# Performance work log

Measured on AMD Instinct MI355X. Metric: run time of the kernel, lower is better.

The kernel has to match this reference:

```python
import jax, jax.numpy as jnp
import numpy as np

B, T, D = 1, 2048, 2048
H, KVH, G, HD = 32, 8, 4, 64  # n_heads, n_kv_heads, n_groups, head_dim


def _rope_angles(t, hd):
    # standard RoPE angle table: [T, hd//2]
    inv_freq = 1.0 / (10000.0 ** (jnp.arange(0, hd, 2, dtype=jnp.float32) / hd))
    return jnp.arange(t, dtype=jnp.float32)[:, None] * inv_freq[None, :]


def setup_inputs() -> dict:
    key = jax.random.key(0)
    k1, k2, k3, k4, k5 = jax.random.split(key, 5)
    scale = 0.02
    return {
        "x": jax.random.normal(k1, (B, T, D), dtype=jnp.float32),
        "freqs": _rope_angles(T, HD),                                  # [T, HD//2]
        "wq": jax.random.normal(k2, (D, H * HD), dtype=jnp.float32) * scale,
        "wk": jax.random.normal(k3, (D, KVH * HD), dtype=jnp.float32) * scale,
        "wv": jax.random.normal(k4, (D, KVH * HD), dtype=jnp.float32) * scale,
        "wo": jax.random.normal(k5, (H * HD, D), dtype=jnp.float32) * scale,
    }


def _apply_rope(t, cos, sin):
    # t: [B, T, nh, HD]; cos/sin: [T, HD//2] -> broadcast [1, T, 1, HD//2]
    t1, t2 = t[..., ::2], t[..., 1::2]
    c = cos[None, :, None, :]
    s = sin[None, :, None, :]
    out_even = t1 * c - t2 * s
    out_odd = t1 * s + t2 * c
    return jnp.stack([out_even, out_odd], axis=-1).reshape(t.shape)


def reference(x, freqs, wq, wk, wv, wo):
    b, t, _ = x.shape
    q = (x @ wq).reshape(b, t, H, HD)
    k = (x @ wk).reshape(b, t, KVH, HD)
    v = (x @ wv).reshape(b, t, KVH, HD)

    cos, sin = jnp.cos(freqs), jnp.sin(freqs)
    q = _apply_rope(q, cos, sin)
    k = _apply_rope(k, cos, sin)

    # GQA: repeat_interleave along head dim (kv head h -> query heads h*G..h*G+G-1)
    k = jnp.repeat(k, G, axis=2)  # [b, t, H, HD]
    v = jnp.repeat(v, G, axis=2)

    scale = 1.0 / jnp.sqrt(jnp.asarray(HD, dtype=x.dtype))
    scores = jnp.einsum("bthd,bshd->bhts", q, k) * scale  # [b, H, t, t]
    causal = jnp.tril(jnp.ones((t, t), dtype=bool))
    scores = jnp.where(causal[None, None], scores, jnp.asarray(-jnp.inf, dtype=scores.dtype))
    attn = jax.nn.softmax(scores, axis=-1)

    out = jnp.einsum("bhts,bshd->bthd", attn, v).reshape(b, t, H * HD)
    return out @ wo
```

## Files before the change

### kernel.cpp

```cpp
#include <hip/hip_runtime.h>
#include <cstdint>
#include <cstddef>

#define T_SEQ 2048
#define D_MODEL 2048
#define NH 32
#define NKVH 8
#define HDIM 64

typedef _Float16 f16;
typedef __attribute__((ext_vector_type(8))) _Float16 half8;
typedef __attribute__((ext_vector_type(4))) _Float16 half4;
typedef __attribute__((ext_vector_type(4))) float floatx4;

#define QSCALE 0.1803368801111204f

#if __has_builtin(__builtin_amdgcn_exp2f)
#define EXP2F(x) __builtin_amdgcn_exp2f(x)
#else
#define EXP2F(x) exp2f(x)
#endif


__device__ __forceinline__ void gload_lds16(const void* g, void* l) {
  __builtin_amdgcn_global_load_lds(
      (const __attribute__((address_space(1))) void*)g,
      (__attribute__((address_space(3))) void*)l,
      16, 0, 0);
}

__global__ __launch_bounds__(256) void prep_kernel(const float* __restrict__ x,
                                                   const float* __restrict__ wq,
                                                   const float* __restrict__ wk,
                                                   const float* __restrict__ wv,
                                                   const float* __restrict__ wo,
                                                   f16* __restrict__ xb,
                                                   f16* __restrict__ wcatT,
                                                   f16* __restrict__ woT) {
  __shared__ f16 tile[64 * 65];
  int tid = threadIdx.x;
  int bx = blockIdx.x;
  if (bx < 4096) {
    int id = bx * 256 + tid;
    int t = id >> 9;
    int d0 = (id & 511) * 4;
    float4 v = ((const float4*)x)[id];
    half4 o;
    o[0] = (f16)v.x; o[1] = (f16)v.y; o[2] = (f16)v.z; o[3] = (f16)v.w;
    int bm = t >> 7, mtb = (t & 127) >> 4, l15 = t & 15;
    int kt = d0 >> 6, s = (d0 & 63) >> 5, quad = (d0 & 31) >> 3, j = d0 & 7;
    size_t off = ((size_t)bm * 32 + kt) * 8192 + mtb * 1024 + s * 512 + (quad * 16 + l15) * 8 + j;
    *(half4*)&xb[off] = o;
    return;
  }
  const float* in;
  f16* out;
  int N, outN0, inCol0, kt;
  if (bx < 5632) {
    int b2 = bx - 4096;
    kt = b2 / 48;
    int cx = b2 - kt * 48;
    out = wcatT;
    if (cx < 32)      { in = wq; N = 2048; outN0 = 0;    inCol0 = cx * 64; }
    else if (cx < 40) { in = wk; N = 512;  outN0 = 2048; inCol0 = (cx - 32) * 64; }
    else              { in = wv; N = 512;  outN0 = 2560; inCol0 = (cx - 40) * 64; }
  } else {
    int b3 = bx - 5632;
    kt = b3 >> 5;
    in = wo; out = woT; N = 2048; outN0 = 0; inCol0 = (b3 & 31) * 64;
  }
  int k0 = kt * 64;
#pragma unroll
  for (int i = 0; i < 16; i++) {
    int idx = i * 256 + tid;
    int kk = idx >> 6, nn = idx & 63;
    tile[nn * 65 + kk] = (f16)in[(size_t)(k0 + kk) * N + inCol0 + nn];
  }
  __syncthreads();
#pragma unroll
  for (int i = 0; i < 2; i++) {
    int idx = i * 256 + tid;
    int dd = idx >> 3, c = idx & 7;
    half8 v8 = *(const half8*)&tile[dd * 65 + c * 8];
    int ng = outN0 + inCol0 + dd;
    int bn = ng >> 7, ntb = (ng & 127) >> 4, l15 = ng & 15;
    int s = c >> 2, quad = c & 3;
    *(half8*)&out[((size_t)bn * 32 + kt) * 8192 + ntb * 1024 + s * 512 + (quad * 16 + l15) * 8] = v8;
  }
}

template <typename OutT>
__global__ __launch_bounds__(256) void gemm_f16_kernel(const f16* __restrict__ A,
                                                       const f16* __restrict__ BT,
                                                       OutT* __restrict__ C,
                                                       int M, int N, int K) {
  __shared__ alignas(16) f16 As[2][4096];
  __shared__ alignas(16) f16 Bs[2][8192];
  int tid = threadIdx.x;
  int wave = tid >> 6, lane = tid & 63;
  int ln15 = lane & 15, quad = lane >> 4;
  int wr = wave >> 1, wc = wave & 1;
  int bm = blockIdx.y, bn = blockIdx.x;
  int ktiles = K >> 6;
  const f16* Ab = A + ((size_t)(bm >> 1) * ktiles) * 8192 + (bm & 1) * 4096;
  const f16* Bb = BT + (size_t)bn * ktiles * 8192;
  floatx4 acc[2][4];
  floatx4 zero = {0.f, 0.f, 0.f, 0.f};
#pragma unroll
  for (int mt = 0; mt < 2; mt++)
#pragma unroll
    for (int nt = 0; nt < 4; nt++) acc[mt][nt] = zero;

  auto stageg = [&](int kt, int buf) {
    const f16* at = Ab + (size_t)kt * 8192;
    const f16* bt = Bb + (size_t)kt * 8192;
#pragma unroll
    for (int i = 0; i < 2; i++)
      gload_lds16(at + (wave * 2 + i) * 512 + lane * 8, &As[buf][(wave * 2 + i) * 512]);
#pragma unroll
    for (int i = 0; i < 4; i++)
      gload_lds16(bt + (wave * 4 + i) * 512 + lane * 8, &Bs[buf][(wave * 4 + i) * 512]);
  };

  stageg(0, 0);
  for (int kt = 0; kt < ktiles; kt++) {
    int cur = kt & 1;
    if (kt + 1 < ktiles) {
      stageg(kt + 1, cur ^ 1);
      asm volatile("s_waitcnt vmcnt(6)\n\ts_barrier" ::: "memory");
    } else {
      asm volatile("s_waitcnt vmcnt(0)\n\ts_barrier" ::: "memory");
    }
#pragma unroll
    for (int s = 0; s < 2; s++) {
      half8 af[2], bf[4];
#pragma unroll
      for (int mt = 0; mt < 2; mt++)
        af[mt] = *(const half8*)&As[cur][(wr * 2 + mt) * 1024 + s * 512 + lane * 8];
#pragma unroll
      for (int nt = 0; nt < 4; nt++)
        bf[nt] = *(const half8*)&Bs[cur][(wc * 4 + nt) * 1024 + s * 512 + lane * 8];
#pragma unroll
      for (int mt = 0; mt < 2; mt++)
#pragma unroll
        for (int nt = 0; nt < 4; nt++)
          acc[mt][nt] = __builtin_amdgcn_mfma_f32_16x16x32_f16(af[mt], bf[nt], acc[mt][nt], 0, 0, 0);
    }
    if (kt + 1 < ktiles) {
      asm volatile("s_waitcnt lgkmcnt(0)\n\ts_barrier" ::: "memory");
    }
  }
  size_t rbase = (size_t)bm * 64 + wr * 32;
  int cbase = bn * 128 + wc * 64;
#pragma unroll
  for (int mt = 0; mt < 2; mt++)
#pragma unroll
    for (int nt = 0; nt < 4; nt++)
#pragma unroll
      for (int r = 0; r < 4; r++)
        C[(rbase + mt * 16 + quad * 4 + r) * (size_t)N + cbase + nt * 16 + ln15] =
            (OutT)acc[mt][nt][r];
}

__global__ __launch_bounds__(256) void rope_tv_kernel(const f16* __restrict__ qkv,
                                                      const float* __restrict__ freqs,
                                                      f16* __restrict__ qr,
                                                      f16* __restrict__ katt,
                                                      f16* __restrict__ vatt) {
  __shared__ f16 tile[64 * 65];
  int tid = threadIdx.x;
  int bx = blockIdx.x;
  if (bx < 10240) {
    int id = bx * 256 + tid;
    int t = id / 1280;
    int pr = id - t * 1280;
    int c0 = pr * 2;
    const f16* row = qkv + (size_t)t * 3072;
    if (c0 < 2048) {
      int h = c0 >> 6, p = (c0 & 63) >> 1;
      float ang = freqs[t * 32 + p];
      float s, c;
      __sincosf(ang, &s, &c);
      float t1 = (float)row[c0], t2 = (float)row[c0 + 1];
      f16* dst = qr + ((size_t)h * T_SEQ + t) * 64 + (c0 & 63);
      dst[0] = (f16)((t1 * c - t2 * s) * QSCALE);
      dst[1] = (f16)((t1 * s + t2 * c) * QSCALE);
    } else {
      int cc = c0 - 2048;
      int kh = cc >> 6, p = (cc & 63) >> 1;
      int d = cc & 63;
      float ang = freqs[t * 32 + p];
      float s, c;
      __sincosf(ang, &s, &c);
      float t1 = (float)row[2048 + cc], t2 = (float)row[2048 + cc + 1];
      int jt = t >> 6, nt = (t & 63) >> 4, ln15 = t & 15;
      int sfr = d >> 5, quad = (d & 31) >> 3, j = d & 7;
      f16* dst = katt + ((size_t)kh * 32 + jt) * 4096 + (nt * 2 + sfr) * 512 +
                 (quad * 16 + ln15) * 8 + j;
      dst[0] = (f16)(t1 * c - t2 * s);
      dst[1] = (f16)(t1 * s + t2 * c);
    }
    return;
  }
  int b2 = bx - 10240;
  int head = b2 >> 5, jt = b2 & 31;
  int t0 = jt * 64;
#pragma unroll
  for (int i = 0; i < 16; i++) {
    int idx = i * 256 + tid;
    int tt = idx >> 6, dd = idx & 63;
    tile[dd * 65 + tt] = qkv[(size_t)(t0 + tt) * 3072 + 2560 + head * 64 + dd];
  }
  __syncthreads();
  f16* vtile = vatt + ((size_t)head * 32 + jt) * 4096;
#pragma unroll
  for (int i = 0; i < 2; i++) {
    int idx = i * 256 + tid;
    int dd = idx >> 3, c = idx & 7;
    half8 v8 = *(const half8*)&tile[dd * 65 + c * 8];
    int nt = dd >> 4, sfr = c >> 2, quad = c & 3, ln15 = dd & 15;
    *(half8*)&vtile[(nt * 2 + sfr) * 512 + (quad * 16 + ln15) * 8] = v8;
  }
}

__global__ __launch_bounds__(512, 4) void attn_fwd_kernel(const f16* __restrict__ q,
                                                          const f16* __restrict__ katt,
                                                          const f16* __restrict__ vatt,
                                                          f16* __restrict__ ao) {
  __shared__ alignas(16) f16 Ks[4][4096];
  __shared__ alignas(16) f16 Vs[4][4096];
  __shared__ alignas(16) f16 Pq[8 * 1024];

  int tid = threadIdx.x;
  int lane = tid & 63, w = tid >> 6;
  int g = w >> 2, wl = w & 3;
  int ln15 = lane & 15, quad = lane >> 4;
  int x = blockIdx.x;
  int h = blockIdx.y;
  int kvh = h >> 2;
  int qtA = x, qtB = 31 - x;
  int R = qtB + 1;
  int S = (R + 1) >> 1;
  int qbaseA = qtA * 64 + wl * 16, qbaseB = qtB * 64 + wl * 16;
  int qglobA = qbaseA + ln15, qglobB = qbaseB + ln15;

  const f16* kh = katt + (size_t)kvh * 32 * 4096;
  const f16* vh = vatt + (size_t)kvh * 32 * 4096;
  f16* P = &Pq[w * 1024];

  const f16* qhA = q + ((size_t)h * T_SEQ + qbaseA) * 64;
  const f16* qhB = q + ((size_t)h * T_SEQ + qbaseB) * 64;
  half8 qfA[2], qfB[2];
#pragma unroll
  for (int s = 0; s < 2; s++) {
    qfA[s] = *(const half8*)&qhA[(size_t)ln15 * 64 + s * 32 + quad * 8];
    qfB[s] = *(const half8*)&qhB[(size_t)ln15 * 64 + s * 32 + quad * 8];
  }

  floatx4 oaccA[4], oaccB[4];
  floatx4 zero = {0.f, 0.f, 0.f, 0.f};
#pragma unroll
  for (int nt = 0; nt < 4; nt++) { oaccA[nt] = zero; oaccB[nt] = zero; }
  float lA = 0.f, lB = 0.f;

  auto stage_pair = [&](int s1) {
    int jtw = 2 * s1 + g;
    if (jtw < R) {
      int buf = ((s1 & 1) << 1) | g;
      const f16* kt = kh + (size_t)jtw * 4096;
      const f16* vt = vh + (size_t)jtw * 4096;
      gload_lds16(kt + (wl * 2 + 0) * 512 + lane * 8, &Ks[buf][(wl * 2 + 0) * 512]);
      gload_lds16(kt + (wl * 2 + 1) * 512 + lane * 8, &Ks[buf][(wl * 2 + 1) * 512]);
      gload_lds16(vt + (wl * 2 + 0) * 512 + lane * 8, &Vs[buf][(wl * 2 + 0) * 512]);
      gload_lds16(vt + (wl * 2 + 1) * 512 + lane * 8, &Vs[buf][(wl * 2 + 1) * 512]);
    }
  };

  auto compute_tile = [&](const half8* qf, floatx4* oacc, float& lsum, bool diag,
                          int qglob, int jt, int buf) {
    floatx4 sacc[4];
    __builtin_amdgcn_s_setprio(1);
#pragma unroll
    for (int nt = 0; nt < 4; nt++) {
      half8 kf0 = *(const half8*)&Ks[buf][(nt * 2 + 0) * 512 + lane * 8];
      half8 kf1 = *(const half8*)&Ks[buf][(nt * 2 + 1) * 512 + lane * 8];
      sacc[nt] = __builtin_amdgcn_mfma_f32_16x16x32_f16(kf0, qf[0], zero, 0, 0, 0);
      sacc[nt] = __builtin_amdgcn_mfma_f32_16x16x32_f16(kf1, qf[1], sacc[nt], 0, 0, 0);
    }
    __builtin_amdgcn_s_setprio(0);
    if (diag) {
#pragma unroll
      for (int nt = 0; nt < 4; nt++)
#pragma unroll
        for (int r = 0; r < 4; r++) {
          int keyg = jt * 64 + nt * 16 + quad * 4 + r;
          if (keyg > qglob) sacc[nt][r] = -1e30f;
        }
    }
    float sum = 0.f;
#pragma unroll
    for (int nt = 0; nt < 4; nt++) {
      float p0 = EXP2F(sacc[nt][0]);
      float p1 = EXP2F(sacc[nt][1]);
      float p2 = EXP2F(sacc[nt][2]);
      float p3 = EXP2F(sacc[nt][3]);
      sum += (p0 + p1) + (p2 + p3);
      half4 ph;
      ph[0] = (f16)p0; ph[1] = (f16)p1; ph[2] = (f16)p2; ph[3] = (f16)p3;
      *(half4*)&P[(nt >> 1) * 512 + (((nt & 1) * 2 + (quad >> 1)) * 16 + ln15) * 8 +
                  (quad & 1) * 4] = ph;
    }
    lsum += sum;
    asm volatile("s_waitcnt lgkmcnt(0)" ::: "memory");
    half8 pf0 = *(const half8*)&P[lane * 8];
    half8 pf1 = *(const half8*)&P[512 + lane * 8];
    __builtin_amdgcn_s_setprio(1);
#pragma unroll
    for (int nt = 0; nt < 4; nt++) {
      half8 vf0 = *(const half8*)&Vs[buf][(nt * 2 + 0) * 512 + lane * 8];
      half8 vf1 = *(const half8*)&Vs[buf][(nt * 2 + 1) * 512 + lane * 8];
      oacc[nt] = __builtin_amdgcn_mfma_f32_16x16x32_f16(vf0, pf0, oacc[nt], 0, 0, 0);
      oacc[nt] = __builtin_amdgcn_mfma_f32_16x16x32_f16(vf1, pf1, oacc[nt], 0, 0, 0);
    }
    __builtin_amdgcn_s_setprio(0);
  };

  stage_pair(0);
  for (int s = 0; s < S; s++) {
    int jt = 2 * s + g;
    int buf = ((s & 1) << 1) | g;
    if (s + 1 < S) {
      stage_pair(s + 1);
      if (2 * (s + 1) + g < R)
        asm volatile("s_waitcnt vmcnt(4) lgkmcnt(0)\n\ts_barrier" ::: "memory");
      else
        asm volatile("s_waitcnt vmcnt(0) lgkmcnt(0)\n\ts_barrier" ::: "memory");
    } else {
      asm volatile("s_waitcnt vmcnt(0) lgkmcnt(0)\n\ts_barrier" ::: "memory");
    }
    if (jt < R) {
      if (jt <= qtA) compute_tile(qfA, oaccA, lA, jt == qtA, qglobA, jt, buf);
      compute_tile(qfB, oaccB, lB, jt == qtB, qglobB, jt, buf);
    }
    if (s + 1 < S)
      asm volatile("s_waitcnt lgkmcnt(0)\n\ts_barrier" ::: "memory");
  }

  floatx4* comb4 = (floatx4*)&Ks[0][0];
  float* combf = (float*)&Ks[0][0];
  int cslot = (wl * 64 + lane) * 10;
  asm volatile("s_waitcnt lgkmcnt(0)\n\ts_barrier" ::: "memory");
  if (g == 1) {
#pragma unroll
    for (int nt = 0; nt < 4; nt++) comb4[cslot + nt] = oaccA[nt];
#pragma unroll
    for (int nt = 0; nt < 4; nt++) comb4[cslot + 4 + nt] = oaccB[nt];
    combf[(cslot + 8) * 4 + 0] = lA;
    combf[(cslot + 8) * 4 + 1] = lB;
  }
  asm volatile("s_waitcnt lgkmcnt(0)\n\ts_barrier" ::: "memory");
  if (g == 0) {
#pragma unroll
    for (int nt = 0; nt < 4; nt++) {
      oaccA[nt] += comb4[cslot + nt];
      oaccB[nt] += comb4[cslot + 4 + nt];
    }
    lA += combf[(cslot + 8) * 4 + 0];
    lB += combf[(cslot + 8) * 4 + 1];
    lA += __shfl_xor(lA, 16);
    lA += __shfl_xor(lA, 32);
    lB += __shfl_xor(lB, 16);
    lB += __shfl_xor(lB, 32);
    float invA = 1.f / lA, invB = 1.f / lB;
    size_t abaseA = (((size_t)(qglobA >> 7)) * 32 + h) * 8192 + ((qbaseA & 127) >> 4) * 1024;
    size_t abaseB = (((size_t)(qglobB >> 7)) * 32 + h) * 8192 + ((qbaseB & 127) >> 4) * 1024;
#pragma unroll
    for (int nt = 0; nt < 4; nt++) {
      half4 ovA, ovB;
#pragma unroll
      for (int r = 0; r < 4; r++) {
        ovA[r] = (f16)(oaccA[nt][r] * invA);
        ovB[r] = (f16)(oaccB[nt][r] * invB);
      }
      int sA = nt >> 1;
      int quadA = (nt & 1) * 2 + (quad >> 1);
      int jA = (quad & 1) * 4;
      size_t foff = sA * 512 + (quadA * 16 + ln15) * 8 + jA;
      *(half4*)&ao[abaseA + foff] = ovA;
      *(half4*)&ao[abaseB + foff] = ovB;
    }
  }
}

extern "C" void kernel_launch(void* const* d_in, const int* in_sizes, int n_in,
                              void* d_out, int out_size, void* d_ws, size_t ws_size,
                              hipStream_t stream) {
  (void)in_sizes; (void)n_in; (void)out_size;
  const float* x = (const float*)d_in[0];
  const float* freqs = (const float*)d_in[1];
  const float* wq = (const float*)d_in[2];
  const float* wk = (const float*)d_in[3];
  const float* wv = (const float*)d_in[4];
  const float* wo = (const float*)d_in[5];
  float* out = (float*)d_out;
  char* ws = (char*)d_ws;
  const size_t MB = 1024 * 1024;

  if (ws_size < 36 * MB) return;

  f16* xb = (f16*)(ws);
  f16* qr = (f16*)(ws);
  f16* wcatT = (f16*)(ws + 8 * MB);
  f16* katt = (f16*)(ws + 8 * MB);
  f16* vatt = (f16*)(ws + 10 * MB);
  f16* ao = (f16*)(ws + 20 * MB);
  f16* woT = (f16*)(ws + 28 * MB);
  f16* qkvh = (f16*)d_out;

  prep_kernel<<<6656, 256, 0, stream>>>(x, wq, wk, wv, wo, xb, wcatT, woT);
  gemm_f16_kernel<f16><<<dim3(3072 / 128, 2048 / 64), 256, 0, stream>>>(xb, wcatT, qkvh,
                                                                        2048, 3072, 2048);
  rope_tv_kernel<<<10496, 256, 0, stream>>>(qkvh, freqs, qr, katt, vatt);
  attn_fwd_kernel<<<dim3(16, NH), 512, 0, stream>>>(qr, katt, vatt, ao);
  gemm_f16_kernel<float><<<dim3(2048 / 128, 2048 / 64), 256, 0, stream>>>(ao, woT, out,
                                                                          2048, 2048, 2048);
}
```

Before: 212.2 us.

## Fuse RoPE and K/V relayout into QKV GEMM epilogue

Removes the separate rope/transpose kernel by applying RoPE, Q scaling and the attention-friendly K/V layouts directly in the QKV GEMM epilogue, using lane shuffles to pair even/odd elements. This avoids writing and re-reading the intermediate qkv buffer and one launch. The epilogue now issues scattered scalar f16 stores and per-element sincos, which may reduce store coalescing, and the workspace grows.

```diff
diff --git a/kernel.cpp b/kernel.cpp
--- a/kernel.cpp
+++ b/kernel.cpp
@@ -89,10 +89,14 @@
   }
 }
 
-template <typename OutT>
+template <typename OutT, int EPI>
 __global__ __launch_bounds__(256) void gemm_f16_kernel(const f16* __restrict__ A,
                                                        const f16* __restrict__ BT,
                                                        OutT* __restrict__ C,
+                                                       const float* __restrict__ freqs,
+                                                       f16* __restrict__ qr,
+                                                       f16* __restrict__ katt,
+                                                       f16* __restrict__ vatt,
                                                        int M, int N, int K) {
   __shared__ alignas(16) f16 As[2][4096];
   __shared__ alignas(16) f16 Bs[2][8192];
@@ -152,74 +156,76 @@
   }
   size_t rbase = (size_t)bm * 64 + wr * 32;
   int cbase = bn * 128 + wc * 64;
-#pragma unroll
-  for (int mt = 0; mt < 2; mt++)
-#pragma unroll
-    for (int nt = 0; nt < 4; nt++)
-#pragma unroll
-      for (int r = 0; r < 4; r++)
-        C[(rbase + mt * 16 + quad * 4 + r) * (size_t)N + cbase + nt * 16 + ln15] =
-            (OutT)acc[mt][nt][r];
-}
-
-__global__ __launch_bounds__(256) void rope_tv_kernel(const f16* __restrict__ qkv,
-                                                      const float* __restrict__ freqs,
-                                                      f16* __restrict__ qr,
-                                                      f16* __restrict__ katt,
-                                                      f16* __restrict__ vatt) {
-  __shared__ f16 tile[64 * 65];
-  int tid = threadIdx.x;
-  int bx = blockIdx.x;
-  if (bx < 10240) {
-    int id = bx * 256 + tid;
-    int t = id / 1280;
-    int pr = id - t * 1280;
-    int c0 = pr * 2;
-    const f16* row = qkv + (size_t)t * 3072;
-    if (c0 < 2048) {
-      int h = c0 >> 6, p = (c0 & 63) >> 1;
-      float ang = freqs[t * 32 + p];
-      float s, c;
-      __sincosf(ang, &s, &c);
-      float t1 = (float)row[c0], t2 = (float)row[c0 + 1];
-      f16* dst = qr + ((size_t)h * T_SEQ + t) * 64 + (c0 & 63);
-      dst[0] = (f16)((t1 * c - t2 * s) * QSCALE);
-      dst[1] = (f16)((t1 * s + t2 * c) * QSCALE);
+
+  if constexpr (EPI == 0) {
+#pragma unroll
+    for (int mt = 0; mt < 2; mt++)
+#pragma unroll
+      for (int nt = 0; nt < 4; nt++)
+#pragma unroll
+        for (int r = 0; r < 4; r++)
+          C[(rbase + mt * 16 + quad * 4 + r) * (size_t)N + cbase + nt * 16 + ln15] =
+              (OutT)acc[mt][nt][r];
+  } else {
+    if (cbase < 2048) {
+#pragma unroll
+      for (int mt = 0; mt < 2; mt++)
+#pragma unroll
+        for (int nt = 0; nt < 4; nt++) {
+          int c = cbase + nt * 16 + ln15;
+          int hq = c >> 6, d = c & 63;
+          int p = d >> 1;
+          float sgn = (d & 1) ? 1.f : -1.f;
+#pragma unroll
+          for (int r = 0; r < 4; r++) {
+            int t = (int)rbase + mt * 16 + quad * 4 + r;
+            float val = acc[mt][nt][r];
+            float prt = __shfl_xor(val, 1);
+            float sv, cv;
+            __sincosf(freqs[t * 32 + p], &sv, &cv);
+            float res = (val * cv + sgn * prt * sv) * QSCALE;
+            qr[((size_t)hq * T_SEQ + t) * 64 + d] = (f16)res;
+          }
+        }
+    } else if (cbase < 2560) {
+#pragma unroll
+      for (int mt = 0; mt < 2; mt++)
+#pragma unroll
+        for (int nt = 0; nt < 4; nt++) {
+          int cc = cbase + nt * 16 + ln15 - 2048;
+          int kh = cc >> 6, d = cc & 63;
+          int p = d >> 1;
+          float sgn = (d & 1) ? 1.f : -1.f;
+          int sfr = d >> 5, quadk = (d & 31) >> 3, j = d & 7;
+#pragma unroll
+          for (int r = 0; r < 4; r++) {
+            int t = (int)rbase + mt * 16 + quad * 4 + r;
+            float val = acc[mt][nt][r];
+            float prt = __shfl_xor(val, 1);
+            float sv, cv;
+            __sincosf(freqs[t * 32 + p], &sv, &cv);
+            float res = val * cv + sgn * prt * sv;
+            int jt = t >> 6, ntk = (t & 63) >> 4, l15k = t & 15;
+            katt[((size_t)(kh * 32 + jt)) * 4096 + (ntk * 2 + sfr) * 512 +
+                 (quadk * 16 + l15k) * 8 + j] = (f16)res;
+          }
+        }
     } else {
-      int cc = c0 - 2048;
-      int kh = cc >> 6, p = (cc & 63) >> 1;
-      int d = cc & 63;
-      float ang = freqs[t * 32 + p];
-      float s, c;
-      __sincosf(ang, &s, &c);
-      float t1 = (float)row[2048 + cc], t2 = (float)row[2048 + cc + 1];
-      int jt = t >> 6, nt = (t & 63) >> 4, ln15 = t & 15;
-      int sfr = d >> 5, quad = (d & 31) >> 3, j = d & 7;
-      f16* dst = katt + ((size_t)kh * 32 + jt) * 4096 + (nt * 2 + sfr) * 512 +
-                 (quad * 16 + ln15) * 8 + j;
-      dst[0] = (f16)(t1 * c - t2 * s);
-      dst[1] = (f16)(t1 * s + t2 * c);
-    }
-    return;
-  }
-  int b2 = bx - 10240;
-  int head = b2 >> 5, jt = b2 & 31;
-  int t0 = jt * 64;
-#pragma unroll
-  for (int i = 0; i < 16; i++) {
-    int idx = i * 256 + tid;
-    int tt = idx >> 6, dd = idx & 63;
-    tile[dd * 65 + tt] = qkv[(size_t)(t0 + tt) * 3072 + 2560 + head * 64 + dd];
-  }
-  __syncthreads();
-  f16* vtile = vatt + ((size_t)head * 32 + jt) * 4096;
-#pragma unroll
-  for (int i = 0; i < 2; i++) {
-    int idx = i * 256 + tid;
-    int dd = idx >> 3, c = idx & 7;
-    half8 v8 = *(const half8*)&tile[dd * 65 + c * 8];
-    int nt = dd >> 4, sfr = c >> 2, quad = c & 3, ln15 = dd & 15;
-    *(half8*)&vtile[(nt * 2 + sfr) * 512 + (quad * 16 + ln15) * 8] = v8;
+#pragma unroll
+      for (int mt = 0; mt < 2; mt++)
+#pragma unroll
+        for (int nt = 0; nt < 4; nt++) {
+          int cc = cbase + nt * 16 + ln15 - 2560;
+          int head = cc >> 6, d = cc & 63;
+#pragma unroll
+          for (int r = 0; r < 4; r++) {
+            int t = (int)rbase + mt * 16 + quad * 4 + r;
+            int jt = t >> 6, tl = t & 63;
+            vatt[((size_t)(head * 32 + jt)) * 4096 + (d >> 4) * 1024 + (tl >> 5) * 512 +
+                 (((tl & 31) >> 3) * 16 + (d & 15)) * 8 + (tl & 7)] = (f16)acc[mt][nt][r];
+          }
+        }
+    }
   }
 }
 
@@ -406,22 +412,20 @@
   char* ws = (char*)d_ws;
   const size_t MB = 1024 * 1024;
 
-  if (ws_size < 36 * MB) return;
+  if (ws_size < 48 * MB) return;
 
   f16* xb = (f16*)(ws);
-  f16* qr = (f16*)(ws);
   f16* wcatT = (f16*)(ws + 8 * MB);
-  f16* katt = (f16*)(ws + 8 * MB);
-  f16* vatt = (f16*)(ws + 10 * MB);
   f16* ao = (f16*)(ws + 20 * MB);
   f16* woT = (f16*)(ws + 28 * MB);
-  f16* qkvh = (f16*)d_out;
+  f16* qr = (f16*)(ws + 36 * MB);
+  f16* katt = (f16*)(ws + 44 * MB);
+  f16* vatt = (f16*)(ws + 46 * MB);
 
   prep_kernel<<<6656, 256, 0, stream>>>(x, wq, wk, wv, wo, xb, wcatT, woT);
-  gemm_f16_kernel<f16><<<dim3(3072 / 128, 2048 / 64), 256, 0, stream>>>(xb, wcatT, qkvh,
-                                                                        2048, 3072, 2048);
-  rope_tv_kernel<<<10496, 256, 0, stream>>>(qkvh, freqs, qr, katt, vatt);
+  gemm_f16_kernel<f16, 1><<<dim3(3072 / 128, 2048 / 64), 256, 0, stream>>>(
+      xb, wcatT, (f16*)nullptr, freqs, qr, katt, vatt, 2048, 3072, 2048);
   attn_fwd_kernel<<<dim3(16, NH), 512, 0, stream>>>(qr, katt, vatt, ao);
-  gemm_f16_kernel<float><<<dim3(2048 / 128, 2048 / 64), 256, 0, stream>>>(ao, woT, out,
-                                                                          2048, 2048, 2048);
+  gemm_f16_kernel<float, 0><<<dim3(2048 / 128, 2048 / 64), 256, 0, stream>>>(
+      ao, woT, out, nullptr, nullptr, nullptr, nullptr, 2048, 2048, 2048);
 }
```

New measurement: 199.5 us (median of 2 runs). 6.0% less time.
